# Kernel tuning notes

Hardware: AMD Instinct MI355X
Metric: run time of the kernel (lower is better)

Reference implementation:

```python
import jax, jax.numpy as jnp
import numpy as np

NUM_HEADS = 8
LOCAL_WINDOW = 32


def setup_inputs() -> dict:
    key = jax.random.key(0)
    ks = jax.random.split(key, 5)
    B, T, D = 2, 2048, 512
    s = 1.0 / np.sqrt(D)
    return {
        "x": jax.random.normal(ks[0], (B, T, D), dtype=jnp.float32),
        "Wq": jax.random.normal(ks[1], (D, D), dtype=jnp.float32) * s,
        "bq": jnp.zeros((D,), dtype=jnp.float32),
        "Wk": jax.random.normal(ks[2], (D, D), dtype=jnp.float32) * s,
        "bk": jnp.zeros((D,), dtype=jnp.float32),
        "Wv": jax.random.normal(ks[3], (D, D), dtype=jnp.float32) * s,
        "bv": jnp.zeros((D,), dtype=jnp.float32),
        "Wo": jax.random.normal(ks[4], (D, D), dtype=jnp.float32) * s,
        "bo": jnp.zeros((D,), dtype=jnp.float32),
    }


def reference(x, Wq, bq, Wk, bk, Wv, bv, Wo, bo):
    B, T, D = x.shape
    H = NUM_HEADS
    hd = D // H
    scale = hd ** -0.5
    w = LOCAL_WINDOW

    def proj(W, b):
        # (B,T,D) -> (B,H,T,hd)
        return (x @ W.T + b).reshape(B, T, H, hd).transpose(0, 2, 1, 3)

    q = proj(Wq, bq)
    k = proj(Wk, bk)
    v = proj(Wv, bv)

    scores = jnp.einsum("bhqd,bhkd->bhqk", q, k) * scale  # (B,H,T,T)

    if w < T:
        i = jnp.arange(T)[:, None]
        j = jnp.arange(T)[None, :]
        # row i attends to columns [i - w//2, i + w//2)  (end exclusive)
        allowed = (j >= i - w // 2) & (j < i + w // 2)  # (T,T)
        scores = jnp.where(allowed[None, None], scores, jnp.float32(-jnp.inf))

    attn = jax.nn.softmax(scores, axis=-1)
    out = jnp.einsum("bhqk,bhkd->bhqd", attn, v)  # (B,H,T,hd)
    out = out.transpose(0, 2, 1, 3).reshape(B, T, D)
    return out @ Wo.T + bo
```

## Files before the change

### kernel.cpp

```cpp
#include <hip/hip_runtime.h>

#define B_  2
#define T_  2048
#define D_  512
#define H_  8
#define HD_ 64
#define WHALF_ 16
#define Mtot (B_*T_)
#define QKV_LD 1536

typedef __attribute__((ext_vector_type(8))) short short8;
typedef __attribute__((ext_vector_type(4))) float floatx4;

__device__ __forceinline__ unsigned short f2bf(float f) {
    unsigned u = __float_as_uint(f);
    u = (u + 0x7fffu + ((u >> 16) & 1u)) >> 16;
    return (unsigned short)u;
}

__device__ __forceinline__ void glds16(const unsigned short* g, unsigned short* l) {
    __builtin_amdgcn_global_load_lds(
        (const __attribute__((address_space(1))) void*)g,
        (__attribute__((address_space(3))) void*)l, 16, 0, 0);
}

__global__ __launch_bounds__(256) void cast_all(
    const float* __restrict__ x,
    const float* __restrict__ Wq, const float* __restrict__ Wk,
    const float* __restrict__ Wv, const float* __restrict__ Wo,
    const float* __restrict__ bq, const float* __restrict__ bk,
    const float* __restrict__ bv,
    unsigned short* __restrict__ xb,
    unsigned short* __restrict__ wqkv, unsigned short* __restrict__ wob,
    float* __restrict__ bqkv)
{
    if (blockIdx.x < 2048) {
        int i = blockIdx.x * 256 + threadIdx.x;
        float4 f = ((const float4*)x)[i];
        ushort4 o;
        o.x = f2bf(f.x); o.y = f2bf(f.y); o.z = f2bf(f.z); o.w = f2bf(f.w);
        ((ushort4*)xb)[i] = o;
    } else if (blockIdx.x < 3072) {
        int gid = (blockIdx.x - 2048) * 256 + threadIdx.x;
        int m   = gid >> 16;
        int idx = gid & 0xFFFF;
        const float* src = (m == 0) ? Wq : (m == 1) ? Wk : (m == 2) ? Wv : Wo;
        float4 f = ((const float4*)src)[idx];
        ushort4 o;
        o.x = f2bf(f.x); o.y = f2bf(f.y); o.z = f2bf(f.z); o.w = f2bf(f.w);
        if (m < 3) ((ushort4*)wqkv)[(m << 16) + idx] = o;
        else       ((ushort4*)wob)[idx] = o;
    } else {
        for (int i = threadIdx.x; i < 384; i += 256) {
            const float* src = (i < 128) ? bq : (i < 256) ? bk : bv;
            ((float4*)bqkv)[i] = ((const float4*)src)[i & 127];
        }
    }
}

__global__ __launch_bounds__(256) void gemm_qkv(
    const unsigned short* __restrict__ A, const unsigned short* __restrict__ W,
    const float* __restrict__ bias, unsigned short* __restrict__ C)
{
    __shared__ unsigned short As[128 * 64];
    __shared__ unsigned short Bs[64 * 64];

    const int t  = threadIdx.x;
    const int m0 = blockIdx.x * 128;
    const int n0 = blockIdx.y * 64;
    const int w  = t >> 6, l = t & 63;
    const int quad = l >> 4, lo = l & 15;
    const int wm = w & 1, wn = w >> 1;

    const int lr = l >> 3;
    const int csw = ((l & 7) ^ lr) * 8;
    const unsigned short* Ag[4];
    unsigned short* ldsA[4];
    #pragma unroll
    for (int p = 0; p < 4; ++p) {
        Ag[p] = A + (size_t)(m0 + 32 * w + 8 * p + lr) * 512 + csw;
        ldsA[p] = &As[(32 * w + 8 * p) * 64];
    }
    const unsigned short* Bg[2];
    unsigned short* ldsB[2];
    #pragma unroll
    for (int p = 0; p < 2; ++p) {
        Bg[p] = W + (size_t)(n0 + 16 * w + 8 * p + lr) * 512 + csw;
        ldsB[p] = &Bs[(16 * w + 8 * p) * 64];
    }

    floatx4 acc[4][2];
    #pragma unroll
    for (int i = 0; i < 4; ++i) { acc[i][0] = (floatx4)0.0f; acc[i][1] = (floatx4)0.0f; }

    const int swlo = lo & 7;

    for (int k0 = 0; k0 < 512; k0 += 64) {
        #pragma unroll
        for (int p = 0; p < 4; ++p) glds16(Ag[p] + k0, ldsA[p]);
        #pragma unroll
        for (int p = 0; p < 2; ++p) glds16(Bg[p] + k0, ldsB[p]);
        __syncthreads();

        #pragma unroll
        for (int ks = 0; ks < 2; ++ks) {
            const int cg = ((ks * 4 + quad) ^ swlo) * 8;
            short8 b0 = *(const short8*)(&Bs[(wn * 32 + lo) * 64 + cg]);
            short8 b1 = *(const short8*)(&Bs[(wn * 32 + 16 + lo) * 64 + cg]);
            #pragma unroll
            for (int i = 0; i < 4; ++i) {
                short8 a = *(const short8*)(&As[(wm * 64 + i * 16 + lo) * 64 + cg]);
                acc[i][0] = __builtin_amdgcn_mfma_f32_16x16x32_bf16(a, b0, acc[i][0], 0, 0, 0);
                acc[i][1] = __builtin_amdgcn_mfma_f32_16x16x32_bf16(a, b1, acc[i][1], 0, 0, 0);
            }
        }
        __syncthreads();
    }

    #pragma unroll
    for (int i = 0; i < 4; ++i) {
        int rbase = m0 + wm * 64 + i * 16 + quad * 4;
        #pragma unroll
        for (int j = 0; j < 2; ++j) {
            int col = n0 + wn * 32 + j * 16 + lo;
            float bv = bias[col];
            #pragma unroll
            for (int r = 0; r < 4; ++r)
                C[(size_t)(rbase + r) * QKV_LD + col] = f2bf(acc[i][j][r] + bv);
        }
    }
}

__global__ __launch_bounds__(256) void gemm_out(
    const unsigned short* __restrict__ attb, const unsigned short* __restrict__ wob,
    const float* __restrict__ bo, float* __restrict__ out)
{
    __shared__ unsigned short As[64 * 64];
    __shared__ unsigned short Bs[64 * 64];

    const int t  = threadIdx.x;
    const int m0 = blockIdx.x * 64;
    const int n0 = blockIdx.y * 64;
    const int w  = t >> 6, l = t & 63;
    const int quad = l >> 4, lo = l & 15;

    const int lr = l >> 3;
    const int csw = ((l & 7) ^ lr) * 8;
    const unsigned short* Ag[2]; unsigned short* ldsA[2];
    const unsigned short* Bg[2]; unsigned short* ldsB[2];
    #pragma unroll
    for (int p = 0; p < 2; ++p) {
        Ag[p] = attb + (size_t)(m0 + 16 * w + 8 * p + lr) * 512 + csw;
        ldsA[p] = &As[(16 * w + 8 * p) * 64];
        Bg[p] = wob + (size_t)(n0 + 16 * w + 8 * p + lr) * 512 + csw;
        ldsB[p] = &Bs[(16 * w + 8 * p) * 64];
    }

    floatx4 acc[4];
    #pragma unroll
    for (int j = 0; j < 4; ++j) acc[j] = (floatx4)0.0f;

    const int swlo = lo & 7;

    for (int k0 = 0; k0 < 512; k0 += 64) {
        #pragma unroll
        for (int p = 0; p < 2; ++p) { glds16(Ag[p] + k0, ldsA[p]); glds16(Bg[p] + k0, ldsB[p]); }
        __syncthreads();

        #pragma unroll
        for (int ks = 0; ks < 2; ++ks) {
            const int cg = ((ks * 4 + quad) ^ swlo) * 8;
            short8 a = *(const short8*)(&As[(w * 16 + lo) * 64 + cg]);
            #pragma unroll
            for (int j = 0; j < 4; ++j) {
                short8 b = *(const short8*)(&Bs[(j * 16 + lo) * 64 + cg]);
                acc[j] = __builtin_amdgcn_mfma_f32_16x16x32_bf16(a, b, acc[j], 0, 0, 0);
            }
        }
        __syncthreads();
    }

    #pragma unroll
    for (int j = 0; j < 4; ++j) {
        int col = n0 + j * 16 + lo;
        float bv = bo[col];
        #pragma unroll
        for (int r = 0; r < 4; ++r) {
            int row = m0 + w * 16 + quad * 4 + r;
            out[(size_t)row * 512 + col] = acc[j][r] + bv;
        }
    }
}

#define KR 96
#define QLD 72
#define VLDP 104

__global__ __launch_bounds__(256) void attn_mfma(
    const unsigned short* __restrict__ qkv, unsigned short* __restrict__ att)
{
    __shared__ unsigned short Qs[64][QLD];
    __shared__ unsigned short Ks[KR][QLD];
    __shared__ unsigned short Vt[64][VLDP];
    __shared__ unsigned short Pws[4][16][VLDP];

    const int q0 = blockIdx.x * 64;
    const int bh = blockIdx.y;
    const int b = bh >> 3, h = bh & 7;
    const int t = threadIdx.x;
    const int wq = t >> 6, l = t & 63;
    const int quad = l >> 4, lo = l & 15;

    const size_t baseQ = (size_t)(b * T_) * QKV_LD + h * HD_;

    for (int c = t; c < 512; c += 256) {
        int row = c >> 3, cg = c & 7;
        *(short8*)(&Qs[row][cg * 8]) =
            *(const short8*)(&qkv[baseQ + (size_t)(q0 + row) * QKV_LD + cg * 8]);
    }
    for (int c = t; c < 768; c += 256) {
        int row = c >> 3, cg = c & 7;
        int g = q0 - WHALF_ + row;
        short8 kv = (short8)(short)0;
        if (g >= 0 && g < T_)
            kv = *(const short8*)(&qkv[baseQ + 512 + (size_t)g * QKV_LD + cg * 8]);
        *(short8*)(&Ks[row][cg * 8]) = kv;
    }
    for (int c = t; c < 768; c += 256) {
        int row = c >> 3, cg = c & 7;
        int g = q0 - WHALF_ + row;
        short8 vv = (short8)(short)0;
        if (g >= 0 && g < T_)
            vv = *(const short8*)(&qkv[baseQ + 1024 + (size_t)g * QKV_LD + cg * 8]);
        #pragma unroll
        for (int j = 0; j < 8; ++j) Vt[cg * 8 + j][row] = vv[j];
    }
    __syncthreads();

    floatx4 S[6];
    #pragma unroll
    for (int kt = 0; kt < 6; ++kt) S[kt] = (floatx4)0.0f;
    short8 aq[2];
    #pragma unroll
    for (int ks = 0; ks < 2; ++ks)
        aq[ks] = *(const short8*)(&Qs[wq * 16 + lo][ks * 32 + quad * 8]);
    #pragma unroll
    for (int kt = 0; kt < 6; ++kt) {
        #pragma unroll
        for (int ks = 0; ks < 2; ++ks) {
            short8 bk8 = *(const short8*)(&Ks[kt * 16 + lo][ks * 32 + quad * 8]);
            S[kt] = __builtin_amdgcn_mfma_f32_16x16x32_bf16(aq[ks], bk8, S[kt], 0, 0, 0);
        }
    }

    float inv_r[4];
    #pragma unroll
    for (int r = 0; r < 4; ++r) {
        int qi = q0 + wq * 16 + quad * 4 + r;
        float mx = -1e30f;
        float sv[6]; bool vd[6];
        #pragma unroll
        for (int kt = 0; kt < 6; ++kt) {
            int j = q0 - WHALF_ + kt * 16 + lo;
            bool ok = (j >= qi - WHALF_) && (j < qi + WHALF_) && (j >= 0) && (j < T_);
            float s = S[kt][r] * 0.125f;
            sv[kt] = s; vd[kt] = ok;
            mx = (ok && s > mx) ? s : mx;
        }
        #pragma unroll
        for (int mm = 1; mm < 16; mm <<= 1) mx = fmaxf(mx, __shfl_xor(mx, mm, 16));
        float den = 0.f;
        #pragma unroll
        for (int kt = 0; kt < 6; ++kt) {
            float e = vd[kt] ? __expf(sv[kt] - mx) : 0.f;
            Pws[wq][quad * 4 + r][kt * 16 + lo] = f2bf(e);
            den += e;
        }
        #pragma unroll
        for (int mm = 1; mm < 16; mm <<= 1) den += __shfl_xor(den, mm, 16);
        inv_r[r] = 1.0f / den;
    }
    __syncthreads();

    floatx4 O[4];
    #pragma unroll
    for (int nt = 0; nt < 4; ++nt) O[nt] = (floatx4)0.0f;
    #pragma unroll
    for (int ks = 0; ks < 3; ++ks) {
        short8 ap = *(const short8*)(&Pws[wq][lo][ks * 32 + quad * 8]);
        #pragma unroll
        for (int nt = 0; nt < 4; ++nt) {
            short8 bv8 = *(const short8*)(&Vt[nt * 16 + lo][ks * 32 + quad * 8]);
            O[nt] = __builtin_amdgcn_mfma_f32_16x16x32_bf16(ap, bv8, O[nt], 0, 0, 0);
        }
    }

    #pragma unroll
    for (int r = 0; r < 4; ++r) {
        int qi = q0 + wq * 16 + quad * 4 + r;
        size_t rowb = (size_t)(b * T_ + qi) * D_ + h * HD_;
        #pragma unroll
        for (int nt = 0; nt < 4; ++nt)
            att[rowb + nt * 16 + lo] = f2bf(O[nt][r] * inv_r[r]);
    }
}

extern "C" void kernel_launch(void* const* d_in, const int* in_sizes, int n_in,
                              void* d_out, int out_size, void* d_ws, size_t ws_size,
                              hipStream_t stream) {
    const float* x  = (const float*)d_in[0];
    const float* Wq = (const float*)d_in[1];
    const float* bq = (const float*)d_in[2];
    const float* Wk = (const float*)d_in[3];
    const float* bk = (const float*)d_in[4];
    const float* Wv = (const float*)d_in[5];
    const float* bv = (const float*)d_in[6];
    const float* Wo = (const float*)d_in[7];
    const float* bo = (const float*)d_in[8];
    float* out = (float*)d_out;

    char* ws = (char*)d_ws;
    unsigned short* xb   = (unsigned short*)(ws);
    unsigned short* wqkv = (unsigned short*)(ws +  4194304);
    unsigned short* wob  = (unsigned short*)(ws +  5767168);
    float*          bqkv = (float*)         (ws +  6291456);
    unsigned short* qkvb = (unsigned short*)(ws +  6297600);
    unsigned short* attb = (unsigned short*)(ws + 18880512);

    cast_all<<<3073, 256, 0, stream>>>(x, Wq, Wk, Wv, Wo, bq, bk, bv,
                                       xb, wqkv, wob, bqkv);

    gemm_qkv<<<dim3(Mtot / 128, QKV_LD / 64), 256, 0, stream>>>(
        xb, wqkv, bqkv, qkvb);

    attn_mfma<<<dim3(T_ / 64, B_ * H_), 256, 0, stream>>>(qkvb, attb);

    gemm_out<<<dim3(Mtot / 64, D_ / 64), 256, 0, stream>>>(attb, wob, bo, out);
}
```

Measured before the change: 106.8 us.

## Shrink QKV GEMM tiles, trim attention key tiles per wave, store V row-major

The QKV projection GEMM now uses 64x64 tiles instead of 128x64, doubling the grid to raise parallelism at the cost of less operand reuse. In attention, each wave computes only the 4 key tiles that can fall inside its window instead of all 6, so fewer MFMAs run and the P buffer shrinks. V is stored row-major with vector writes rather than transposed element by element, but the PV B-operand is now gathered with 8 scalar LDS reads per MFMA. One block-wide barrier before PV is removed, since each wave only reads its own P rows.

```diff
diff --git a/kernel.cpp b/kernel.cpp
--- a/kernel.cpp
+++ b/kernel.cpp
@@ -10,6 +10,7 @@
 #define QKV_LD 1536
 
 typedef __attribute__((ext_vector_type(8))) short short8;
+typedef __attribute__((ext_vector_type(4))) short short4v;
 typedef __attribute__((ext_vector_type(4))) float floatx4;
 
 __device__ __forceinline__ unsigned short f2bf(float f) {
@@ -62,79 +63,6 @@
     const unsigned short* __restrict__ A, const unsigned short* __restrict__ W,
     const float* __restrict__ bias, unsigned short* __restrict__ C)
 {
-    __shared__ unsigned short As[128 * 64];
-    __shared__ unsigned short Bs[64 * 64];
-
-    const int t  = threadIdx.x;
-    const int m0 = blockIdx.x * 128;
-    const int n0 = blockIdx.y * 64;
-    const int w  = t >> 6, l = t & 63;
-    const int quad = l >> 4, lo = l & 15;
-    const int wm = w & 1, wn = w >> 1;
-
-    const int lr = l >> 3;
-    const int csw = ((l & 7) ^ lr) * 8;
-    const unsigned short* Ag[4];
-    unsigned short* ldsA[4];
-    #pragma unroll
-    for (int p = 0; p < 4; ++p) {
-        Ag[p] = A + (size_t)(m0 + 32 * w + 8 * p + lr) * 512 + csw;
-        ldsA[p] = &As[(32 * w + 8 * p) * 64];
-    }
-    const unsigned short* Bg[2];
-    unsigned short* ldsB[2];
-    #pragma unroll
-    for (int p = 0; p < 2; ++p) {
-        Bg[p] = W + (size_t)(n0 + 16 * w + 8 * p + lr) * 512 + csw;
-        ldsB[p] = &Bs[(16 * w + 8 * p) * 64];
-    }
-
-    floatx4 acc[4][2];
-    #pragma unroll
-    for (int i = 0; i < 4; ++i) { acc[i][0] = (floatx4)0.0f; acc[i][1] = (floatx4)0.0f; }
-
-    const int swlo = lo & 7;
-
-    for (int k0 = 0; k0 < 512; k0 += 64) {
-        #pragma unroll
-        for (int p = 0; p < 4; ++p) glds16(Ag[p] + k0, ldsA[p]);
-        #pragma unroll
-        for (int p = 0; p < 2; ++p) glds16(Bg[p] + k0, ldsB[p]);
-        __syncthreads();
-
-        #pragma unroll
-        for (int ks = 0; ks < 2; ++ks) {
-            const int cg = ((ks * 4 + quad) ^ swlo) * 8;
-            short8 b0 = *(const short8*)(&Bs[(wn * 32 + lo) * 64 + cg]);
-            short8 b1 = *(const short8*)(&Bs[(wn * 32 + 16 + lo) * 64 + cg]);
-            #pragma unroll
-            for (int i = 0; i < 4; ++i) {
-                short8 a = *(const short8*)(&As[(wm * 64 + i * 16 + lo) * 64 + cg]);
-                acc[i][0] = __builtin_amdgcn_mfma_f32_16x16x32_bf16(a, b0, acc[i][0], 0, 0, 0);
-                acc[i][1] = __builtin_amdgcn_mfma_f32_16x16x32_bf16(a, b1, acc[i][1], 0, 0, 0);
-            }
-        }
-        __syncthreads();
-    }
-
-    #pragma unroll
-    for (int i = 0; i < 4; ++i) {
-        int rbase = m0 + wm * 64 + i * 16 + quad * 4;
-        #pragma unroll
-        for (int j = 0; j < 2; ++j) {
-            int col = n0 + wn * 32 + j * 16 + lo;
-            float bv = bias[col];
-            #pragma unroll
-            for (int r = 0; r < 4; ++r)
-                C[(size_t)(rbase + r) * QKV_LD + col] = f2bf(acc[i][j][r] + bv);
-        }
-    }
-}
-
-__global__ __launch_bounds__(256) void gemm_out(
-    const unsigned short* __restrict__ attb, const unsigned short* __restrict__ wob,
-    const float* __restrict__ bo, float* __restrict__ out)
-{
     __shared__ unsigned short As[64 * 64];
     __shared__ unsigned short Bs[64 * 64];
 
@@ -150,9 +78,9 @@
     const unsigned short* Bg[2]; unsigned short* ldsB[2];
     #pragma unroll
     for (int p = 0; p < 2; ++p) {
-        Ag[p] = attb + (size_t)(m0 + 16 * w + 8 * p + lr) * 512 + csw;
+        Ag[p] = A + (size_t)(m0 + 16 * w + 8 * p + lr) * 512 + csw;
         ldsA[p] = &As[(16 * w + 8 * p) * 64];
-        Bg[p] = wob + (size_t)(n0 + 16 * w + 8 * p + lr) * 512 + csw;
+        Bg[p] = W + (size_t)(n0 + 16 * w + 8 * p + lr) * 512 + csw;
         ldsB[p] = &Bs[(16 * w + 8 * p) * 64];
     }
 
@@ -183,6 +111,67 @@
     #pragma unroll
     for (int j = 0; j < 4; ++j) {
         int col = n0 + j * 16 + lo;
+        float bv = bias[col];
+        #pragma unroll
+        for (int r = 0; r < 4; ++r) {
+            int row = m0 + w * 16 + quad * 4 + r;
+            C[(size_t)row * QKV_LD + col] = f2bf(acc[j][r] + bv);
+        }
+    }
+}
+
+__global__ __launch_bounds__(256) void gemm_out(
+    const unsigned short* __restrict__ attb, const unsigned short* __restrict__ wob,
+    const float* __restrict__ bo, float* __restrict__ out)
+{
+    __shared__ unsigned short As[64 * 64];
+    __shared__ unsigned short Bs[64 * 64];
+
+    const int t  = threadIdx.x;
+    const int m0 = blockIdx.x * 64;
+    const int n0 = blockIdx.y * 64;
+    const int w  = t >> 6, l = t & 63;
+    const int quad = l >> 4, lo = l & 15;
+
+    const int lr = l >> 3;
+    const int csw = ((l & 7) ^ lr) * 8;
+    const unsigned short* Ag[2]; unsigned short* ldsA[2];
+    const unsigned short* Bg[2]; unsigned short* ldsB[2];
+    #pragma unroll
+    for (int p = 0; p < 2; ++p) {
+        Ag[p] = attb + (size_t)(m0 + 16 * w + 8 * p + lr) * 512 + csw;
+        ldsA[p] = &As[(16 * w + 8 * p) * 64];
+        Bg[p] = wob + (size_t)(n0 + 16 * w + 8 * p + lr) * 512 + csw;
+        ldsB[p] = &Bs[(16 * w + 8 * p) * 64];
+    }
+
+    floatx4 acc[4];
+    #pragma unroll
+    for (int j = 0; j < 4; ++j) acc[j] = (floatx4)0.0f;
+
+    const int swlo = lo & 7;
+
+    for (int k0 = 0; k0 < 512; k0 += 64) {
+        #pragma unroll
+        for (int p = 0; p < 2; ++p) { glds16(Ag[p] + k0, ldsA[p]); glds16(Bg[p] + k0, ldsB[p]); }
+        __syncthreads();
+
+        #pragma unroll
+        for (int ks = 0; ks < 2; ++ks) {
+            const int cg = ((ks * 4 + quad) ^ swlo) * 8;
+            short8 a = *(const short8*)(&As[(w * 16 + lo) * 64 + cg]);
+            #pragma unroll
+            for (int j = 0; j < 4; ++j) {
+                short8 b = *(const short8*)(&Bs[(j * 16 + lo) * 64 + cg]);
+                acc[j] = __builtin_amdgcn_mfma_f32_16x16x32_bf16(a, b, acc[j], 0, 0, 0);
+            }
+        }
+        __syncthreads();
+    }
+
+    #pragma unroll
+    for (int j = 0; j < 4; ++j) {
+        int col = n0 + j * 16 + lo;
         float bv = bo[col];
         #pragma unroll
         for (int r = 0; r < 4; ++r) {
@@ -192,17 +181,16 @@
     }
 }
 
-#define KR 96
 #define QLD 72
-#define VLDP 104
+#define VLD 76
 
 __global__ __launch_bounds__(256) void attn_mfma(
     const unsigned short* __restrict__ qkv, unsigned short* __restrict__ att)
 {
     __shared__ unsigned short Qs[64][QLD];
-    __shared__ unsigned short Ks[KR][QLD];
-    __shared__ unsigned short Vt[64][VLDP];
-    __shared__ unsigned short Pws[4][16][VLDP];
+    __shared__ unsigned short Ks[96][QLD];
+    __shared__ unsigned short Vs[96][VLD];
+    __shared__ unsigned short Pws[4][16][QLD];
 
     const int q0 = blockIdx.x * 64;
     const int bh = blockIdx.y;
@@ -232,24 +220,29 @@
         short8 vv = (short8)(short)0;
         if (g >= 0 && g < T_)
             vv = *(const short8*)(&qkv[baseQ + 1024 + (size_t)g * QKV_LD + cg * 8]);
-        #pragma unroll
-        for (int j = 0; j < 8; ++j) Vt[cg * 8 + j][row] = vv[j];
+        short4v lo4 = { vv[0], vv[1], vv[2], vv[3] };
+        short4v hi4 = { vv[4], vv[5], vv[6], vv[7] };
+        *(short4v*)(&Vs[row][cg * 8])     = lo4;
+        *(short4v*)(&Vs[row][cg * 8 + 4]) = hi4;
     }
     __syncthreads();
 
-    floatx4 S[6];
-    #pragma unroll
-    for (int kt = 0; kt < 6; ++kt) S[kt] = (floatx4)0.0f;
+    const int ks0 = wq >> 1;
+    const int kb  = ks0 * 2;
+
+    floatx4 S[4];
+    #pragma unroll
+    for (int tt = 0; tt < 4; ++tt) S[tt] = (floatx4)0.0f;
     short8 aq[2];
     #pragma unroll
     for (int ks = 0; ks < 2; ++ks)
         aq[ks] = *(const short8*)(&Qs[wq * 16 + lo][ks * 32 + quad * 8]);
     #pragma unroll
-    for (int kt = 0; kt < 6; ++kt) {
+    for (int tt = 0; tt < 4; ++tt) {
         #pragma unroll
         for (int ks = 0; ks < 2; ++ks) {
-            short8 bk8 = *(const short8*)(&Ks[kt * 16 + lo][ks * 32 + quad * 8]);
-            S[kt] = __builtin_amdgcn_mfma_f32_16x16x32_bf16(aq[ks], bk8, S[kt], 0, 0, 0);
+            short8 bk8 = *(const short8*)(&Ks[(kb + tt) * 16 + lo][ks * 32 + quad * 8]);
+            S[tt] = __builtin_amdgcn_mfma_f32_16x16x32_bf16(aq[ks], bk8, S[tt], 0, 0, 0);
         }
     }
 
@@ -258,39 +251,42 @@
     for (int r = 0; r < 4; ++r) {
         int qi = q0 + wq * 16 + quad * 4 + r;
         float mx = -1e30f;
-        float sv[6]; bool vd[6];
-        #pragma unroll
-        for (int kt = 0; kt < 6; ++kt) {
-            int j = q0 - WHALF_ + kt * 16 + lo;
+        float sv[4]; bool vd[4];
+        #pragma unroll
+        for (int tt = 0; tt < 4; ++tt) {
+            int j = q0 - WHALF_ + (kb + tt) * 16 + lo;
             bool ok = (j >= qi - WHALF_) && (j < qi + WHALF_) && (j >= 0) && (j < T_);
-            float s = S[kt][r] * 0.125f;
-            sv[kt] = s; vd[kt] = ok;
+            float s = S[tt][r] * 0.125f;
+            sv[tt] = s; vd[tt] = ok;
             mx = (ok && s > mx) ? s : mx;
         }
         #pragma unroll
         for (int mm = 1; mm < 16; mm <<= 1) mx = fmaxf(mx, __shfl_xor(mx, mm, 16));
         float den = 0.f;
         #pragma unroll
-        for (int kt = 0; kt < 6; ++kt) {
-            float e = vd[kt] ? __expf(sv[kt] - mx) : 0.f;
-            Pws[wq][quad * 4 + r][kt * 16 + lo] = f2bf(e);
+        for (int tt = 0; tt < 4; ++tt) {
+            float e = vd[tt] ? __expf(sv[tt] - mx) : 0.f;
+            Pws[wq][quad * 4 + r][tt * 16 + lo] = f2bf(e);
             den += e;
         }
         #pragma unroll
         for (int mm = 1; mm < 16; mm <<= 1) den += __shfl_xor(den, mm, 16);
         inv_r[r] = 1.0f / den;
     }
-    __syncthreads();
 
     floatx4 O[4];
     #pragma unroll
     for (int nt = 0; nt < 4; ++nt) O[nt] = (floatx4)0.0f;
     #pragma unroll
-    for (int ks = 0; ks < 3; ++ks) {
-        short8 ap = *(const short8*)(&Pws[wq][lo][ks * 32 + quad * 8]);
+    for (int ksr = 0; ksr < 2; ++ksr) {
+        short8 ap = *(const short8*)(&Pws[wq][lo][ksr * 32 + quad * 8]);
+        const int krow = (ks0 + ksr) * 32 + quad * 8;
         #pragma unroll
         for (int nt = 0; nt < 4; ++nt) {
-            short8 bv8 = *(const short8*)(&Vt[nt * 16 + lo][ks * 32 + quad * 8]);
+            short8 bv8;
+            #pragma unroll
+            for (int j = 0; j < 8; ++j)
+                bv8[j] = (short)Vs[krow + j][nt * 16 + lo];
             O[nt] = __builtin_amdgcn_mfma_f32_16x16x32_bf16(ap, bv8, O[nt], 0, 0, 0);
         }
     }
@@ -330,7 +326,7 @@
     cast_all<<<3073, 256, 0, stream>>>(x, Wq, Wk, Wv, Wo, bq, bk, bv,
                                        xb, wqkv, wob, bqkv);
 
-    gemm_qkv<<<dim3(Mtot / 128, QKV_LD / 64), 256, 0, stream>>>(
+    gemm_qkv<<<dim3(Mtot / 64, QKV_LD / 64), 256, 0, stream>>>(
         xb, wqkv, bqkv, qkvb);
 
     attn_mfma<<<dim3(T_ / 64, B_ * H_), 256, 0, stream>>>(qkvb, attb);
```

New measurement: 106.0 us (median of 2 runs). No clear change (-0.7%).
